# Performance work log

Measured on AMD Instinct MI355X. Metric: run time of the kernel, lower is better.

Reference implementation:

```python
import jax, jax.numpy as jnp
import numpy as np

N_GRAPHS = 64


def gcn_conv(x, W, b, src, dst, n_nodes):
    """PyG GCNConv: add self-loops, symmetric D^-1/2 (A+I) D^-1/2 normalization,
    linear transform, scatter-add aggregation at target nodes, plus bias."""
    xw = x @ W  # [N, out]  transform before propagate (PyG order)
    loop = jnp.arange(n_nodes, dtype=src.dtype)
    rows = jnp.concatenate([src, loop])  # message sources
    cols = jnp.concatenate([dst, loop])  # message targets
    deg = jax.ops.segment_sum(jnp.ones_like(cols, dtype=xw.dtype), cols,
                              num_segments=n_nodes)
    dinv = jnp.where(deg > 0, jax.lax.rsqrt(deg), 0.0)
    norm = dinv[rows] * dinv[cols]  # [E+N]
    msgs = norm[:, None] * xw[rows]  # gather + scale
    out = jax.ops.segment_sum(msgs, cols, num_segments=n_nodes)  # scatter-add
    return out + b


def global_mean_pool(x, batch, n_graphs):
    sums = jax.ops.segment_sum(x, batch, num_segments=n_graphs)
    cnts = jax.ops.segment_sum(jnp.ones((x.shape[0],), x.dtype), batch,
                               num_segments=n_graphs)
    return sums / jnp.maximum(cnts, 1.0)[:, None]


def setup_inputs() -> dict:
    key = jax.random.key(0)
    k1, k2, k3, k4, k5, k6 = jax.random.split(key, 6)
    N, E = 50000, 800000
    d_in, d_hid, d_out = 128, 128, 64
    x = jax.random.normal(k1, (N, d_in), dtype=jnp.float32)
    edge_index = jax.random.randint(k2, (2, E), 0, N, dtype=jnp.int64)
    batch = jnp.sort(jax.random.randint(k3, (N,), 0, N_GRAPHS, dtype=jnp.int64))
    # Glorot-ish init for GCN weights, zero bias (PyG default)
    W1 = jax.random.normal(k4, (d_in, d_hid), dtype=jnp.float32) / np.sqrt(d_in)
    b1 = jnp.zeros((d_hid,), jnp.float32)
    W2 = jax.random.normal(k5, (d_hid, d_out), dtype=jnp.float32) / np.sqrt(d_hid)
    b2 = jnp.zeros((d_out,), jnp.float32)
    return {"x": x, "edge_index": edge_index, "batch": batch,
            "W1": W1, "b1": b1, "W2": W2, "b2": b2}


def reference(x, edge_index, batch, W1, b1, W2, b2):
    n_nodes = x.shape[0]
    src, dst = edge_index[0], edge_index[1]
    h = jax.nn.relu(gcn_conv(x, W1, b1, src, dst, n_nodes))
    h = gcn_conv(h, W2, b2, src, dst, n_nodes)
    return global_mean_pool(h, batch, N_GRAPHS)
```

## Files before the change

### kernel.cpp

```cpp
#include <hip/hip_runtime.h>

typedef __attribute__((ext_vector_type(8))) short bf16x8;
typedef __attribute__((ext_vector_type(4))) float f32x4;

__device__ __forceinline__ unsigned short f2bf(float f) {
  unsigned u = __float_as_uint(f);
  u += 0x7FFFu + ((u >> 16) & 1u);
  return (unsigned short)(u >> 16);
}
__device__ __forceinline__ float bflo(unsigned u) { return __uint_as_float(u << 16); }
__device__ __forceinline__ float bfhi(unsigned u) { return __uint_as_float(u & 0xFFFF0000u); }

template <int CO, bool AF32, int RT>
__device__ __forceinline__ void gemm_body(const void* __restrict__ Aptr,
                                          const float* __restrict__ W,
                                          const float* __restrict__ dinv,
                                          unsigned short* __restrict__ Y, int N,
                                          int bid, int tid, unsigned short* Wl) {
  constexpr int K = 128;
  constexpr int SP = K + 8;
  for (int i = tid; i < K * CO; i += 256) {
    int k = i / CO, n = i % CO;
    Wl[n * SP + k] = f2bf(W[i]);
  }
  __syncthreads();

  const int lane = tid & 63;
  const int quad = lane >> 4, l16 = lane & 15;

#pragma unroll
  for (int rt = 0; rt < RT; rt++) {
    const int mbase = bid * (64 * RT) + rt * 64 + (tid >> 6) * 16;
    const int arow = min(mbase + l16, N - 1);

    bf16x8 afrag[4];
    if constexpr (AF32) {
      const float* A = (const float*)Aptr + (size_t)arow * K;
#pragma unroll
      for (int ks = 0; ks < 4; ks++) {
        const float4* p = (const float4*)(A + ks * 32 + quad * 8);
        float4 f0 = p[0], f1 = p[1];
        afrag[ks] = (bf16x8){(short)f2bf(f0.x), (short)f2bf(f0.y), (short)f2bf(f0.z), (short)f2bf(f0.w),
                             (short)f2bf(f1.x), (short)f2bf(f1.y), (short)f2bf(f1.z), (short)f2bf(f1.w)};
      }
    } else {
      const unsigned short* A = (const unsigned short*)Aptr + (size_t)arow * K;
#pragma unroll
      for (int ks = 0; ks < 4; ks++) afrag[ks] = *(const bf16x8*)(A + ks * 32 + quad * 8);
    }

    float dvr[4];
#pragma unroll
    for (int reg = 0; reg < 4; reg++) {
      int node = mbase + quad * 4 + reg;
      dvr[reg] = (node < N) ? dinv[node] : 0.0f;
    }

#pragma unroll
    for (int ct = 0; ct < CO / 16; ct++) {
      f32x4 acc = {0.0f, 0.0f, 0.0f, 0.0f};
#pragma unroll
      for (int ks = 0; ks < 4; ks++) {
        bf16x8 b = *(const bf16x8*)(&Wl[(ct * 16 + l16) * SP + ks * 32 + quad * 8]);
        acc = __builtin_amdgcn_mfma_f32_16x16x32_bf16(afrag[ks], b, acc, 0, 0, 0);
      }
#pragma unroll
      for (int reg = 0; reg < 4; reg++) {
        int node = mbase + quad * 4 + reg;
        if (node < N) Y[(size_t)node * CO + ct * 16 + l16] = f2bf(acc[reg] * dvr[reg]);
        else if (node == N) Y[(size_t)node * CO + ct * 16 + l16] = 0;
      }
    }
  }
}

__global__ __launch_bounds__(256) void k_hist(const int* __restrict__ dst,
                                              int* __restrict__ cnt,
                                              int* __restrict__ rank, int E) {
  const int e0 = (blockIdx.x * 256 + threadIdx.x) * 4;
  if (e0 + 3 < E) {
    int4 d4 = *(const int4*)(dst + e0);
    int4 r;
    r.x = atomicAdd(&cnt[d4.x], 1);
    r.y = atomicAdd(&cnt[d4.y], 1);
    r.z = atomicAdd(&cnt[d4.z], 1);
    r.w = atomicAdd(&cnt[d4.w], 1);
    *(int4*)(rank + e0) = r;
  } else {
    for (int e = e0; e < E; e++) rank[e] = atomicAdd(&cnt[dst[e]], 1);
  }
}

__global__ void k_seg(const int* __restrict__ cnt, int* __restrict__ start,
                      float* __restrict__ dinv, int* __restrict__ counter,
                      const int* __restrict__ batch, int* __restrict__ firstIdx, int N) {
  const int v = blockIdx.x * 256 + threadIdx.x;
  const int lane = threadIdx.x & 63;
  if (v < N) {
    int b = batch[v];
    if (v == 0 || batch[v - 1] != b) firstIdx[b] = v + 1;
  }
  int c = (v < N) ? cnt[v] : 0;
  int incl = c;
#pragma unroll
  for (int d = 1; d < 64; d <<= 1) {
    int t = __shfl_up(incl, d, 64);
    if (lane >= d) incl += t;
  }
  int base = 0;
  if (lane == 63) base = atomicAdd(counter, incl);
  base = __shfl(base, 63, 64);
  if (v < N) {
    start[v] = base + incl - c;
    dinv[v] = rsqrtf((float)(c + 1));
  }
}

__global__ __launch_bounds__(256) void k_gemm1(const float* __restrict__ x,
                                               const float* __restrict__ W1,
                                               const float* __restrict__ dinv,
                                               unsigned short* __restrict__ Y, int N) {
  __shared__ unsigned short Wl[128 * 136];
  gemm_body<128, true, 4>(x, W1, dinv, Y, N, blockIdx.x, threadIdx.x, Wl);
}

__global__ void k_fill(const int* __restrict__ src, const int* __restrict__ dst,
                       const int* __restrict__ rank, const int* __restrict__ start,
                       unsigned short* __restrict__ colw16, int E) {
  int e = blockIdx.x * 256 + threadIdx.x;
  if (e < E) {
    int s = src[e], d = dst[e];
    colw16[start[d] + rank[e]] = (unsigned short)s;
  }
}

__global__ __launch_bounds__(256) void k_agg128(const unsigned short* __restrict__ xwb,
                                                const float* __restrict__ dinv,
                                                const int* __restrict__ start,
                                                const int* __restrict__ cnt,
                                                const unsigned short* __restrict__ colw16,
                                                const float* __restrict__ bias,
                                                unsigned short* __restrict__ out, int N) {
  const int tid = threadIdx.x;
  const int lane = tid & 63;
  const int gl = lane & 15;
  const int grp = lane >> 4;
  const int wv = tid >> 6;
  const int v = blockIdx.x * 16 + wv * 4 + grp;
  const int vc = min(v, N - 1);

  const float dv = dinv[vc];
  const int j0 = start[vc];
  const int jc = (v < N) ? cnt[vc] : 0;

  float acc[8];
  {
    uint4 s = *(const uint4*)((const char*)xwb + (((size_t)vc << 8) | (gl << 4)));
    acc[0] = bflo(s.x); acc[1] = bfhi(s.x);
    acc[2] = bflo(s.y); acc[3] = bfhi(s.y);
    acc[4] = bflo(s.z); acc[5] = bfhi(s.z);
    acc[6] = bflo(s.w); acc[7] = bfhi(s.w);
  }

  const int gbase = grp << 4;
  for (int base = 0; __any(base < jc); base += 16) {
    int cs = (base + gl < jc) ? (int)colw16[j0 + base + gl] : N;
    int mv = jc - base;
    mv = mv < 0 ? 0 : (mv > 16 ? 16 : mv);
    int mm = max(mv, __shfl_xor(mv, 16, 64));
    mm = max(mm, __shfl_xor(mm, 32, 64));
    const int rp = (mm + 3) & ~3;
    for (int t = 0; t < rp; t += 4) {
      uint4 rbuf[4];
#pragma unroll
      for (int r = 0; r < 4; r++) {
        int sx = __shfl(cs, gbase + t + r, 64);
        rbuf[r] = *(const uint4*)((const char*)xwb + (((unsigned)sx << 8) | (gl << 4)));
      }
#pragma unroll
      for (int r = 0; r < 4; r++) {
        const uint4 rr = rbuf[r];
        acc[0] += bflo(rr.x); acc[1] += bfhi(rr.x);
        acc[2] += bflo(rr.y); acc[3] += bfhi(rr.y);
        acc[4] += bflo(rr.z); acc[5] += bfhi(rr.z);
        acc[6] += bflo(rr.w); acc[7] += bfhi(rr.w);
      }
    }
  }

  if (v < N) {
    float4 b0 = ((const float4*)bias)[gl * 2];
    float4 b1 = ((const float4*)bias)[gl * 2 + 1];
    float a0 = fmaxf(dv * acc[0] + b0.x, 0.f), a1 = fmaxf(dv * acc[1] + b0.y, 0.f);
    float a2 = fmaxf(dv * acc[2] + b0.z, 0.f), a3 = fmaxf(dv * acc[3] + b0.w, 0.f);
    float a4 = fmaxf(dv * acc[4] + b1.x, 0.f), a5 = fmaxf(dv * acc[5] + b1.y, 0.f);
    float a6 = fmaxf(dv * acc[6] + b1.z, 0.f), a7 = fmaxf(dv * acc[7] + b1.w, 0.f);
    uint4 st;
    st.x = (unsigned)f2bf(a0) | ((unsigned)f2bf(a1) << 16);
    st.y = (unsigned)f2bf(a2) | ((unsigned)f2bf(a3) << 16);
    st.z = (unsigned)f2bf(a4) | ((unsigned)f2bf(a5) << 16);
    st.w = (unsigned)f2bf(a6) | ((unsigned)f2bf(a7) << 16);
    *(uint4*)((char*)out + (((size_t)v << 8) | (gl << 4))) = st;
  }
}

__global__ __launch_bounds__(256) void k_gemm2(const unsigned short* __restrict__ A,
                                               const float* __restrict__ W,
                                               const float* __restrict__ dinv,
                                               unsigned short* __restrict__ Y, int N) {
  __shared__ unsigned short Wl[64 * 136];
  gemm_body<64, false, 4>(A, W, dinv, Y, N, blockIdx.x, threadIdx.x, Wl);
}

__global__ __launch_bounds__(256) void k_aggpool(const unsigned short* __restrict__ xwb,
                                                 const float* __restrict__ dinv,
                                                 const int* __restrict__ start,
                                                 const int* __restrict__ cnt,
                                                 const unsigned short* __restrict__ colw16,
                                                 const int* __restrict__ batch,
                                                 float* __restrict__ stage, int N) {
  __shared__ float sAcc[4][64];
  const int tid = threadIdx.x;
  const int lane = tid & 63;
  const int gl = lane & 7;
  const int grp = lane >> 3;
  const int wv = tid >> 6;
  const int v = blockIdx.x * 32 + wv * 8 + grp;
  const int vc = min(v, N - 1);

  const float dv = (v < N) ? dinv[vc] : 0.0f;
  const int j0 = start[vc];
  const int jc = (v < N) ? cnt[vc] : 0;
  const int b = batch[vc];

  float acc[8];
  {
    uint4 s = *(const uint4*)((const char*)xwb + (((size_t)vc << 7) | (gl << 4)));
    acc[0] = bflo(s.x); acc[1] = bfhi(s.x);
    acc[2] = bflo(s.y); acc[3] = bfhi(s.y);
    acc[4] = bflo(s.z); acc[5] = bfhi(s.z);
    acc[6] = bflo(s.w); acc[7] = bfhi(s.w);
  }

  const int gbase = grp << 3;
  for (int base = 0; __any(base < jc); base += 8) {
    int cs = (base + gl < jc) ? (int)colw16[j0 + base + gl] : N;
    int mv = jc - base;
    mv = mv < 0 ? 0 : (mv > 8 ? 8 : mv);
    int mm = max(mv, __shfl_xor(mv, 8, 64));
    mm = max(mm, __shfl_xor(mm, 16, 64));
    mm = max(mm, __shfl_xor(mm, 32, 64));
    const int rp = (mm + 3) & ~3;
    for (int t = 0; t < rp; t += 4) {
      uint4 rbuf[4];
#pragma unroll
      for (int r = 0; r < 4; r++) {
        int sx = __shfl(cs, gbase + t + r, 64);
        rbuf[r] = *(const uint4*)((const char*)xwb + (((unsigned)sx << 7) | (gl << 4)));
      }
#pragma unroll
      for (int r = 0; r < 4; r++) {
        const uint4 rr = rbuf[r];
        acc[0] += bflo(rr.x); acc[1] += bfhi(rr.x);
        acc[2] += bflo(rr.y); acc[3] += bfhi(rr.y);
        acc[4] += bflo(rr.z); acc[5] += bfhi(rr.z);
        acc[6] += bflo(rr.w); acc[7] += bfhi(rr.w);
      }
    }
  }

#pragma unroll
  for (int k = 0; k < 8; k++) acc[k] *= dv;

  const int v0 = blockIdx.x * 32;
  const bool uniform = (v0 + 31 < N) && (batch[v0] == batch[v0 + 31]);
  if (uniform) {
#pragma unroll
    for (int d = 8; d < 64; d <<= 1)
#pragma unroll
      for (int k = 0; k < 8; k++) acc[k] += __shfl_xor(acc[k], d, 64);
    if (grp == 0) {
      *(float4*)&sAcc[wv][gl * 8] = make_float4(acc[0], acc[1], acc[2], acc[3]);
      *(float4*)&sAcc[wv][gl * 8 + 4] = make_float4(acc[4], acc[5], acc[6], acc[7]);
    }
    __syncthreads();
    if (wv == 0) {
      float t = sAcc[0][lane] + sAcc[1][lane] + sAcc[2][lane] + sAcc[3][lane];
      atomicAdd(&stage[batch[v0] * 64 + lane], t);
    }
  } else if (v < N) {
#pragma unroll
    for (int k = 0; k < 8; k++) atomicAdd(&stage[b * 64 + gl * 8 + k], acc[k]);
  }
}

__global__ void k_final(const float* __restrict__ stage, const int* __restrict__ firstIdx,
                        const float* __restrict__ b2, float* __restrict__ out, int N) {
  __shared__ float denom[64];
  const int tid = threadIdx.x;
  if (tid < 64) {
    int raw = firstIdx[tid];
    int fi = (raw > 0) ? raw - 1 : 0x7FFFFFFF;
    int m = fi;
#pragma unroll
    for (int d = 1; d < 64; d <<= 1) {
      int t = __shfl_down(m, d, 64);
      if (tid + d < 64) m = min(m, t);
    }
    int nxtm = __shfl_down(m, 1, 64);
    int nxt = (tid == 63) ? N : min(nxtm, N);
    int c = (fi == 0x7FFFFFFF) ? 0 : (nxt - fi);
    denom[tid] = fmaxf((float)c, 1.0f);
  }
  __syncthreads();
  for (int i = tid; i < 64 * 64; i += 256)
    out[i] = stage[i] / denom[i >> 6] + b2[i & 63];
}


extern "C" void kernel_launch(void* const* d_in, const int* in_sizes, int n_in,
                              void* d_out, int out_size, void* d_ws, size_t ws_size,
                              hipStream_t stream) {
  const float* x     = (const float*)d_in[0];
  const int*   ei    = (const int*)d_in[1];
  const int*   batch = (const int*)d_in[2];
  const float* W1    = (const float*)d_in[3];
  const float* b1    = (const float*)d_in[4];
  const float* W2    = (const float*)d_in[5];
  const float* b2    = (const float*)d_in[6];

  const int N = in_sizes[2];
  const int E = in_sizes[1] / 2;
  const int* src  = ei;
  const int* dstv = ei + E;

  unsigned short* xw1b = (unsigned short*)d_ws;
  unsigned short* h1b  = xw1b + (size_t)(N + 1) * 128;
  unsigned short* xw2b = xw1b;
  int*   cnt     = (int*)(h1b + (size_t)N * 128);
  int*   counter = cnt + N;
  int*   firstIdx= counter + 1;
  float* stage   = (float*)(firstIdx + 64);
  int*   startv  = (int*)(stage + 4096);
  float* dinv    = (float*)(startv + N);
  int*   rank    = (int*)(((uintptr_t)(dinv + N) + 15) & ~(uintptr_t)15);
  unsigned short* colw16 = (unsigned short*)(rank + E);
  float* outp    = (float*)d_out;

  hipMemsetAsync(cnt, 0, (size_t)(N + 1 + 64 + 4096) * sizeof(int), stream);

  const int gM  = (N + 255) / 256;
  const int gE4 = (E + 1023) / 1024;
  const int gE  = (E + 255) / 256;
  const int gN  = (N + 255) / 256;
  const int gA1 = (N + 15) / 16;
  const int gA2 = (N + 31) / 32;

  k_hist<<<gE4, 256, 0, stream>>>(dstv, cnt, rank, E);
  k_seg<<<gN, 256, 0, stream>>>(cnt, startv, dinv, counter, batch, firstIdx, N);
  k_gemm1<<<gM, 256, 0, stream>>>(x, W1, dinv, xw1b, N);
  k_fill<<<gE, 256, 0, stream>>>(src, dstv, rank, startv, colw16, E);

  k_agg128<<<gA1, 256, 0, stream>>>(xw1b, dinv, startv, cnt, colw16, b1, h1b, N);

  k_gemm2<<<gM, 256, 0, stream>>>(h1b, W2, dinv, xw2b, N);
  k_aggpool<<<gA2, 256, 0, stream>>>(xw2b, dinv, startv, cnt, colw16, batch, stage, N);

  k_final<<<1, 256, 0, stream>>>(stage, firstIdx, b2, outp, N);
}
```

Baseline: 227.2 us.

## Fuse scan into GEMM1 launch, fold final pooling into aggpool, drop dinv buffer

Result: no change. 228.7 us (+0.6%).

```diff
diff --git a/kernel.cpp b/kernel.cpp
--- a/kernel.cpp
+++ b/kernel.cpp
@@ -14,7 +14,7 @@
 template <int CO, bool AF32, int RT>
 __device__ __forceinline__ void gemm_body(const void* __restrict__ Aptr,
                                           const float* __restrict__ W,
-                                          const float* __restrict__ dinv,
+                                          const int* __restrict__ cnt,
                                           unsigned short* __restrict__ Y, int N,
                                           int bid, int tid, unsigned short* Wl) {
   constexpr int K = 128;
@@ -53,7 +53,7 @@
 #pragma unroll
     for (int reg = 0; reg < 4; reg++) {
       int node = mbase + quad * 4 + reg;
-      dvr[reg] = (node < N) ? dinv[node] : 0.0f;
+      dvr[reg] = (node < N) ? rsqrtf((float)(cnt[node] + 1)) : 0.0f;
     }
 
 #pragma unroll
@@ -91,43 +91,65 @@
   }
 }
 
-__global__ void k_seg(const int* __restrict__ cnt, int* __restrict__ start,
-                      float* __restrict__ dinv, int* __restrict__ counter,
-                      const int* __restrict__ batch, int* __restrict__ firstIdx, int N) {
-  const int v = blockIdx.x * 256 + threadIdx.x;
-  const int lane = threadIdx.x & 63;
-  if (v < N) {
-    int b = batch[v];
-    if (v == 0 || batch[v - 1] != b) firstIdx[b] = v + 1;
-  }
-  int c = (v < N) ? cnt[v] : 0;
-  int incl = c;
-#pragma unroll
-  for (int d = 1; d < 64; d <<= 1) {
-    int t = __shfl_up(incl, d, 64);
-    if (lane >= d) incl += t;
-  }
-  int base = 0;
-  if (lane == 63) base = atomicAdd(counter, incl);
-  base = __shfl(base, 63, 64);
-  if (v < N) {
-    start[v] = base + incl - c;
-    dinv[v] = rsqrtf((float)(c + 1));
-  }
-}
-
-__global__ __launch_bounds__(256) void k_gemm1(const float* __restrict__ x,
-                                               const float* __restrict__ W1,
-                                               const float* __restrict__ dinv,
-                                               unsigned short* __restrict__ Y, int N) {
+__global__ __launch_bounds__(256) void k_mega(const float* __restrict__ x,
+                                              const float* __restrict__ W1,
+                                              const int* __restrict__ cnt,
+                                              unsigned short* __restrict__ xw1b, int N,
+                                              int* __restrict__ start,
+                                              int* __restrict__ counter,
+                                              const int* __restrict__ batch,
+                                              int* __restrict__ firstIdx, int gM) {
   __shared__ unsigned short Wl[128 * 136];
-  gemm_body<128, true, 4>(x, W1, dinv, Y, N, blockIdx.x, threadIdx.x, Wl);
+  const int bid = blockIdx.x, tid = threadIdx.x;
+  if (bid < gM) {
+    gemm_body<128, true, 4>(x, W1, cnt, xw1b, N, bid, tid, Wl);
+  } else {
+    const int v = (bid - gM) * 256 + tid;
+    const int lane = tid & 63;
+    if (v < N) {
+      int b = batch[v];
+      if (v == 0 || batch[v - 1] != b) firstIdx[b] = v + 1;
+    }
+    int c = (v < N) ? cnt[v] : 0;
+    int incl = c;
+#pragma unroll
+    for (int d = 1; d < 64; d <<= 1) {
+      int t = __shfl_up(incl, d, 64);
+      if (lane >= d) incl += t;
+    }
+    int base = 0;
+    if (lane == 63) base = atomicAdd(counter, incl);
+    base = __shfl(base, 63, 64);
+    if (v < N) start[v] = base + incl - c;
+  }
 }
 
 __global__ void k_fill(const int* __restrict__ src, const int* __restrict__ dst,
                        const int* __restrict__ rank, const int* __restrict__ start,
-                       unsigned short* __restrict__ colw16, int E) {
-  int e = blockIdx.x * 256 + threadIdx.x;
+                       unsigned short* __restrict__ colw16, int E,
+                       const int* __restrict__ firstIdx, const float* __restrict__ b2,
+                       float* __restrict__ invc, float* __restrict__ out, int N, int gE) {
+  const int bid = blockIdx.x;
+  const int tid = threadIdx.x;
+  if (bid == gE) {
+    if (tid < 64) {
+      int raw = firstIdx[tid];
+      int fi = (raw > 0) ? raw - 1 : 0x7FFFFFFF;
+      int m = fi;
+#pragma unroll
+      for (int d = 1; d < 64; d <<= 1) {
+        int t = __shfl_down(m, d, 64);
+        if (tid + d < 64) m = min(m, t);
+      }
+      int nxtm = __shfl_down(m, 1, 64);
+      int nxt = (tid == 63) ? N : min(nxtm, N);
+      int c = (fi == 0x7FFFFFFF) ? 0 : (nxt - fi);
+      invc[tid] = 1.0f / fmaxf((float)c, 1.0f);
+    }
+    for (int i = tid; i < 64 * 64; i += 256) out[i] = b2[i & 63];
+    return;
+  }
+  int e = bid * 256 + tid;
   if (e < E) {
     int s = src[e], d = dst[e];
     colw16[start[d] + rank[e]] = (unsigned short)s;
@@ -135,7 +157,6 @@
 }
 
 __global__ __launch_bounds__(256) void k_agg128(const unsigned short* __restrict__ xwb,
-                                                const float* __restrict__ dinv,
                                                 const int* __restrict__ start,
                                                 const int* __restrict__ cnt,
                                                 const unsigned short* __restrict__ colw16,
@@ -149,9 +170,9 @@
   const int v = blockIdx.x * 16 + wv * 4 + grp;
   const int vc = min(v, N - 1);
 
-  const float dv = dinv[vc];
   const int j0 = start[vc];
   const int jc = (v < N) ? cnt[vc] : 0;
+  const float dv = rsqrtf((float)(jc + 1));
 
   float acc[8];
   {
@@ -169,16 +190,16 @@
     mv = mv < 0 ? 0 : (mv > 16 ? 16 : mv);
     int mm = max(mv, __shfl_xor(mv, 16, 64));
     mm = max(mm, __shfl_xor(mm, 32, 64));
-    const int rp = (mm + 3) & ~3;
-    for (int t = 0; t < rp; t += 4) {
-      uint4 rbuf[4];
-#pragma unroll
-      for (int r = 0; r < 4; r++) {
+    const int rp = (mm + 7) & ~7;
+    for (int t = 0; t < rp; t += 8) {
+      uint4 rbuf[8];
+#pragma unroll
+      for (int r = 0; r < 8; r++) {
         int sx = __shfl(cs, gbase + t + r, 64);
         rbuf[r] = *(const uint4*)((const char*)xwb + (((unsigned)sx << 8) | (gl << 4)));
       }
 #pragma unroll
-      for (int r = 0; r < 4; r++) {
+      for (int r = 0; r < 8; r++) {
         const uint4 rr = rbuf[r];
         acc[0] += bflo(rr.x); acc[1] += bfhi(rr.x);
         acc[2] += bflo(rr.y); acc[3] += bfhi(rr.y);
@@ -206,19 +227,19 @@
 
 __global__ __launch_bounds__(256) void k_gemm2(const unsigned short* __restrict__ A,
                                                const float* __restrict__ W,
-                                               const float* __restrict__ dinv,
+                                               const int* __restrict__ cnt,
                                                unsigned short* __restrict__ Y, int N) {
   __shared__ unsigned short Wl[64 * 136];
-  gemm_body<64, false, 4>(A, W, dinv, Y, N, blockIdx.x, threadIdx.x, Wl);
+  gemm_body<64, false, 4>(A, W, cnt, Y, N, blockIdx.x, threadIdx.x, Wl);
 }
 
 __global__ __launch_bounds__(256) void k_aggpool(const unsigned short* __restrict__ xwb,
-                                                 const float* __restrict__ dinv,
                                                  const int* __restrict__ start,
                                                  const int* __restrict__ cnt,
                                                  const unsigned short* __restrict__ colw16,
                                                  const int* __restrict__ batch,
-                                                 float* __restrict__ stage, int N) {
+                                                 const float* __restrict__ invc,
+                                                 float* __restrict__ out, int N) {
   __shared__ float sAcc[4][64];
   const int tid = threadIdx.x;
   const int lane = tid & 63;
@@ -228,9 +249,9 @@
   const int v = blockIdx.x * 32 + wv * 8 + grp;
   const int vc = min(v, N - 1);
 
-  const float dv = (v < N) ? dinv[vc] : 0.0f;
   const int j0 = start[vc];
   const int jc = (v < N) ? cnt[vc] : 0;
+  const float dv = (v < N) ? rsqrtf((float)(jc + 1)) : 0.0f;
   const int b = batch[vc];
 
   float acc[8];
@@ -245,32 +266,25 @@
   const int gbase = grp << 3;
   for (int base = 0; __any(base < jc); base += 8) {
     int cs = (base + gl < jc) ? (int)colw16[j0 + base + gl] : N;
-    int mv = jc - base;
-    mv = mv < 0 ? 0 : (mv > 8 ? 8 : mv);
-    int mm = max(mv, __shfl_xor(mv, 8, 64));
-    mm = max(mm, __shfl_xor(mm, 16, 64));
-    mm = max(mm, __shfl_xor(mm, 32, 64));
-    const int rp = (mm + 3) & ~3;
-    for (int t = 0; t < rp; t += 4) {
-      uint4 rbuf[4];
-#pragma unroll
-      for (int r = 0; r < 4; r++) {
-        int sx = __shfl(cs, gbase + t + r, 64);
-        rbuf[r] = *(const uint4*)((const char*)xwb + (((unsigned)sx << 7) | (gl << 4)));
-      }
-#pragma unroll
-      for (int r = 0; r < 4; r++) {
-        const uint4 rr = rbuf[r];
-        acc[0] += bflo(rr.x); acc[1] += bfhi(rr.x);
-        acc[2] += bflo(rr.y); acc[3] += bfhi(rr.y);
-        acc[4] += bflo(rr.z); acc[5] += bfhi(rr.z);
-        acc[6] += bflo(rr.w); acc[7] += bfhi(rr.w);
-      }
-    }
-  }
-
-#pragma unroll
-  for (int k = 0; k < 8; k++) acc[k] *= dv;
+    uint4 rbuf[8];
+#pragma unroll
+    for (int r = 0; r < 8; r++) {
+      int sx = __shfl(cs, gbase + r, 64);
+      rbuf[r] = *(const uint4*)((const char*)xwb + (((unsigned)sx << 7) | (gl << 4)));
+    }
+#pragma unroll
+    for (int r = 0; r < 8; r++) {
+      const uint4 rr = rbuf[r];
+      acc[0] += bflo(rr.x); acc[1] += bfhi(rr.x);
+      acc[2] += bflo(rr.y); acc[3] += bfhi(rr.y);
+      acc[4] += bflo(rr.z); acc[5] += bfhi(rr.z);
+      acc[6] += bflo(rr.w); acc[7] += bfhi(rr.w);
+    }
+  }
+
+  const float sc = dv * invc[b];
+#pragma unroll
+  for (int k = 0; k < 8; k++) acc[k] *= sc;
 
   const int v0 = blockIdx.x * 32;
   const bool uniform = (v0 + 31 < N) && (batch[v0] == batch[v0 + 31]);
@@ -286,35 +300,12 @@
     __syncthreads();
     if (wv == 0) {
       float t = sAcc[0][lane] + sAcc[1][lane] + sAcc[2][lane] + sAcc[3][lane];
-      atomicAdd(&stage[batch[v0] * 64 + lane], t);
+      atomicAdd(&out[batch[v0] * 64 + lane], t);
     }
   } else if (v < N) {
 #pragma unroll
-    for (int k = 0; k < 8; k++) atomicAdd(&stage[b * 64 + gl * 8 + k], acc[k]);
-  }
-}
-
-__global__ void k_final(const float* __restrict__ stage, const int* __restrict__ firstIdx,
-                        const float* __restrict__ b2, float* __restrict__ out, int N) {
-  __shared__ float denom[64];
-  const int tid = threadIdx.x;
-  if (tid < 64) {
-    int raw = firstIdx[tid];
-    int fi = (raw > 0) ? raw - 1 : 0x7FFFFFFF;
-    int m = fi;
-#pragma unroll
-    for (int d = 1; d < 64; d <<= 1) {
-      int t = __shfl_down(m, d, 64);
-      if (tid + d < 64) m = min(m, t);
-    }
-    int nxtm = __shfl_down(m, 1, 64);
-    int nxt = (tid == 63) ? N : min(nxtm, N);
-    int c = (fi == 0x7FFFFFFF) ? 0 : (nxt - fi);
-    denom[tid] = fmaxf((float)c, 1.0f);
-  }
-  __syncthreads();
-  for (int i = tid; i < 64 * 64; i += 256)
-    out[i] = stage[i] / denom[i >> 6] + b2[i & 63];
+    for (int k = 0; k < 8; k++) atomicAdd(&out[b * 64 + gl * 8 + k], acc[k]);
+  }
 }
 
 
@@ -340,14 +331,13 @@
   int*   cnt     = (int*)(h1b + (size_t)N * 128);
   int*   counter = cnt + N;
   int*   firstIdx= counter + 1;
-  float* stage   = (float*)(firstIdx + 64);
-  int*   startv  = (int*)(stage + 4096);
-  float* dinv    = (float*)(startv + N);
-  int*   rank    = (int*)(((uintptr_t)(dinv + N) + 15) & ~(uintptr_t)15);
+  float* invc    = (float*)(firstIdx + 64);
+  int*   startv  = (int*)(invc + 64);
+  int*   rank    = (int*)(((uintptr_t)(startv + N) + 15) & ~(uintptr_t)15);
   unsigned short* colw16 = (unsigned short*)(rank + E);
   float* outp    = (float*)d_out;
 
-  hipMemsetAsync(cnt, 0, (size_t)(N + 1 + 64 + 4096) * sizeof(int), stream);
+  hipMemsetAsync(cnt, 0, (size_t)(N + 1 + 64) * sizeof(int), stream);
 
   const int gM  = (N + 255) / 256;
   const int gE4 = (E + 1023) / 1024;
@@ -357,14 +347,13 @@
   const int gA2 = (N + 31) / 32;
 
   k_hist<<<gE4, 256, 0, stream>>>(dstv, cnt, rank, E);
-  k_seg<<<gN, 256, 0, stream>>>(cnt, startv, dinv, counter, batch, firstIdx, N);
-  k_gemm1<<<gM, 256, 0, stream>>>(x, W1, dinv, xw1b, N);
-  k_fill<<<gE, 256, 0, stream>>>(src, dstv, rank, startv, colw16, E);
-
-  k_agg128<<<gA1, 256, 0, stream>>>(xw1b, dinv, startv, cnt, colw16, b1, h1b, N);
-
-  k_gemm2<<<gM, 256, 0, stream>>>(h1b, W2, dinv, xw2b, N);
-  k_aggpool<<<gA2, 256, 0, stream>>>(xw2b, dinv, startv, cnt, colw16, batch, stage, N);
-
-  k_final<<<1, 256, 0, stream>>>(stage, firstIdx, b2, outp, N);
-}
+  k_mega<<<gM + gN, 256, 0, stream>>>(x, W1, cnt, xw1b, N, startv, counter,
+                                      batch, firstIdx, gM);
+  k_fill<<<gE + 1, 256, 0, stream>>>(src, dstv, rank, startv, colw16, E,
+                                     firstIdx, b2, invc, outp, N, gE);
+
+  k_agg128<<<gA1, 256, 0, stream>>>(xw1b, startv, cnt, colw16, b1, h1b, N);
+
+  k_gemm2<<<gM, 256, 0, stream>>>(h1b, W2, cnt, xw2b, N);
+  k_aggpool<<<gA2, 256, 0, stream>>>(xw2b, startv, cnt, colw16, batch, invc, outp, N);
+}
```
